# Kernel tuning notes

Hardware: AMD Instinct MI355X
Metric: run time of the kernel (lower is better)

## Reference

```python
import jax, jax.numpy as jnp
import numpy as np

B, S, D, H = 2, 2048, 2048, 16
HD = D // H
QMAX = 127.0  # 8-bit activation quant


def ste_round(x):
    # forward: round; backward: identity
    return x + jax.lax.stop_gradient(jnp.round(x) - x)


def bitlinear(x, w):
    """BitNet b1.58 linear: per-tensor ternary weights + per-token int8 activations.

    x: [..., in], w: [out, in] -> [..., out]
    """
    w_scale = jnp.maximum(jnp.mean(jnp.abs(w)), 1e-6)
    w_q = jnp.clip(ste_round(w / w_scale), -1.0, 1.0)          # ternary {-1,0,1}
    a_max = jnp.clip(jnp.max(jnp.abs(x), axis=-1, keepdims=True), 1e-8, None)
    x_q = jnp.clip(ste_round(x * (QMAX / a_max)), -QMAX, QMAX)  # int8 range
    y = jnp.einsum('bsi,oi->bso', x_q, w_q)
    return y * (w_scale * a_max / QMAX)


def setup_inputs() -> dict:
    key = jax.random.key(0)
    ks = jax.random.split(key, 5)
    std = 1.0 / np.sqrt(D)  # muP-style init from BitLinear
    return {
        'x': jax.random.normal(ks[0], (B, S, D), dtype=jnp.float32),
        'wq': jax.random.normal(ks[1], (D, D), dtype=jnp.float32) * std,
        'wk': jax.random.normal(ks[2], (D, D), dtype=jnp.float32) * std,
        'wv': jax.random.normal(ks[3], (D, D), dtype=jnp.float32) * std,
        'wo': jax.random.normal(ks[4], (D, D), dtype=jnp.float32) * std,
    }


def reference(x, wq, wk, wv, wo):
    q = bitlinear(x, wq).reshape(B, S, H, HD)
    k = bitlinear(x, wk).reshape(B, S, H, HD)
    v = bitlinear(x, wv).reshape(B, S, H, HD)
    scores = jnp.einsum('bqhd,bkhd->bhqk', q, k) / np.sqrt(HD)
    # causal mask
    causal = jnp.tril(jnp.ones((S, S), dtype=bool))
    scores = jnp.where(causal[None, None], scores, jnp.finfo(scores.dtype).min)
    attn = jax.nn.softmax(scores, axis=-1)
    ctx = jnp.einsum('bhqk,bkhd->bqhd', attn, v).reshape(B, S, D)
    return bitlinear(ctx, wo)
```

## Files before the change

kernel.cpp:

```cpp
#include <hip/hip_runtime.h>
#include <hip/hip_bf16.h>
#include <cstdint>
#include <cstddef>


#define BB 2
#define SS 2048
#define DD 2048
#define HH 16
#define HDD 128
#define MM (BB*SS)

typedef __attribute__((ext_vector_type(8))) short bf16x8;
typedef __attribute__((ext_vector_type(4))) float f32x4;
typedef __attribute__((ext_vector_type(16))) float f32x16;
typedef __attribute__((ext_vector_type(4))) int   i32x4;
typedef unsigned short u16;
typedef unsigned int   u32;
typedef unsigned char  u8;
typedef signed char    s8;

#define MFMA(a,b,c)   __builtin_amdgcn_mfma_f32_16x16x32_bf16(a,b,c,0,0,0)
#define MFMA32(a,b,c) __builtin_amdgcn_mfma_f32_32x32x16_bf16(a,b,c,0,0,0)
#define MFMAI8(a,b,c) __builtin_amdgcn_mfma_i32_16x16x64_i8(a,b,c,0,0,0)

static __device__ __forceinline__ u16 f2bf(float f) {
  u32 x = __float_as_uint(f);
  u32 r = x + 0x7fffu + ((x >> 16) & 1u);
  return (u16)(r >> 16);
}

static __device__ __forceinline__ u32 cvtpk(float a, float b) {
  u32 r;
  asm("v_cvt_pk_bf16_f32 %0, %1, %2" : "=v"(r) : "v"(a), "v"(b));
  return r;
}

static __device__ __forceinline__ void gl_lds16(const void* g, void* l) {
  __builtin_amdgcn_global_load_lds((const __attribute__((address_space(1))) void*)g,
                                   (__attribute__((address_space(3))) void*)l, 16, 0, 0);
}

__global__ __launch_bounds__(256) void k_prep(const float* __restrict__ x, s8* __restrict__ xq,
                                              float* __restrict__ amax,
                                              const float* __restrict__ w0, const float* __restrict__ w1,
                                              const float* __restrict__ w2, const float* __restrict__ w3,
                                              double* __restrict__ part) {
  __shared__ double redd[256];
  __shared__ float  redf[4];
  int t = threadIdx.x;
  if (blockIdx.x < MM) {
    int row = blockIdx.x;
    const float* p = x + (size_t)row * DD + t * 8;
    float4 v0 = *(const float4*)(p);
    float4 v1 = *(const float4*)(p + 4);
    float f[8];
    f[0] = v0.x; f[1] = v0.y; f[2] = v0.z; f[3] = v0.w;
    f[4] = v1.x; f[5] = v1.y; f[6] = v1.z; f[7] = v1.w;
    float m = 0.f;
    #pragma unroll
    for (int i = 0; i < 8; i++) m = fmaxf(m, fabsf(f[i]));
    m = fmaxf(m, __shfl_xor(m, 1));  m = fmaxf(m, __shfl_xor(m, 2));
    m = fmaxf(m, __shfl_xor(m, 4));  m = fmaxf(m, __shfl_xor(m, 8));
    m = fmaxf(m, __shfl_xor(m, 16)); m = fmaxf(m, __shfl_xor(m, 32));
    if ((t & 63) == 0) redf[t >> 6] = m;
    __syncthreads();
    m = fmaxf(fmaxf(redf[0], redf[1]), fmaxf(redf[2], redf[3]));
    m = fmaxf(m, 1e-8f);
    if (t == 0) amax[row] = m;
    float s = 127.0f / m;
    s8 o[8];
    #pragma unroll
    for (int i = 0; i < 8; i++)
      o[i] = (s8)(int)fminf(127.f, fmaxf(-127.f, rintf(f[i] * s)));
    *(uint2*)(xq + (size_t)row * DD + t * 8) = *(const uint2*)o;
  } else {
    int idx = blockIdx.x - MM;
    int m = idx >> 8, blk = idx & 255;
    const float* w = (m == 0) ? w0 : (m == 1) ? w1 : (m == 2) ? w2 : w3;
    const float* p = w + (size_t)blk * 16384;
    double s = 0.0;
    for (int i = t * 4; i < 16384; i += 1024) {
      float4 v = *(const float4*)(p + i);
      s += (double)fabsf(v.x) + (double)fabsf(v.y) + (double)fabsf(v.z) + (double)fabsf(v.w);
    }
    redd[t] = s;
    __syncthreads();
    for (int off = 128; off > 0; off >>= 1) {
      if (t < off) redd[t] += redd[t + off];
      __syncthreads();
    }
    if (t == 0) part[m * 256 + blk] = redd[0];
  }
}

__global__ void k_wscale_final(const double* __restrict__ part, float* __restrict__ scales) {
  int m = threadIdx.x;
  if (m < 4) {
    double s = 0.0;
    for (int i = 0; i < 256; i++) s += part[m * 256 + i];
    float v = (float)(s * (1.0 / 4194304.0));
    scales[m] = fmaxf(v, 1e-6f);
  }
}

__global__ void k_wquant(const float* __restrict__ w0, const float* __restrict__ w1,
                         const float* __restrict__ w2, const float* __restrict__ w3,
                         s8* __restrict__ wq, const float* __restrict__ scales) {
  int m = blockIdx.y;
  const float* w = (m == 0) ? w0 : (m == 1) ? w1 : (m == 2) ? w2 : w3;
  float ws = scales[m];
  size_t i = ((size_t)blockIdx.x * 256 + threadIdx.x) * 4;
  float4 v = *(const float4*)(w + i);
  s8 o[4];
  o[0] = (s8)(int)fminf(1.f, fmaxf(-1.f, rintf(v.x / ws)));
  o[1] = (s8)(int)fminf(1.f, fmaxf(-1.f, rintf(v.y / ws)));
  o[2] = (s8)(int)fminf(1.f, fmaxf(-1.f, rintf(v.z / ws)));
  o[3] = (s8)(int)fminf(1.f, fmaxf(-1.f, rintf(v.w / ws)));
  *(int*)(wq + (size_t)m * DD * DD + i) = *(const int*)o;
}

__global__ __launch_bounds__(256) void k_rowquant_bf(const u16* __restrict__ xin, s8* __restrict__ xq,
                                                     float* __restrict__ amax) {
  int row = blockIdx.x, t = threadIdx.x;
  const u16* p = xin + (size_t)row * DD + t * 8;
  int4 v = *(const int4*)p;
  const u16* pv = (const u16*)&v;
  float f[8];
  #pragma unroll
  for (int i = 0; i < 8; i++) f[i] = __uint_as_float((u32)pv[i] << 16);
  float m = 0.f;
  #pragma unroll
  for (int i = 0; i < 8; i++) m = fmaxf(m, fabsf(f[i]));
  m = fmaxf(m, __shfl_xor(m, 1));  m = fmaxf(m, __shfl_xor(m, 2));
  m = fmaxf(m, __shfl_xor(m, 4));  m = fmaxf(m, __shfl_xor(m, 8));
  m = fmaxf(m, __shfl_xor(m, 16)); m = fmaxf(m, __shfl_xor(m, 32));
  __shared__ float red[4];
  if ((t & 63) == 0) red[t >> 6] = m;
  __syncthreads();
  m = fmaxf(fmaxf(red[0], red[1]), fmaxf(red[2], red[3]));
  m = fmaxf(m, 1e-8f);
  if (t == 0) amax[row] = m;
  float s = 127.0f / m;
  s8 o[8];
  #pragma unroll
  for (int i = 0; i < 8; i++)
    o[i] = (s8)(int)fminf(127.f, fmaxf(-127.f, rintf(f[i] * s)));
  *(uint2*)(xq + (size_t)row * DD + t * 8) = *(const uint2*)o;
}

template<bool OB, int NBNL, int BN>
__global__ __launch_bounds__(512) void k_gemm(const s8* __restrict__ A, const s8* __restrict__ Bw,
                                              const float* __restrict__ amax,
                                              const float* __restrict__ scales, int sbase,
                                              void* __restrict__ outv) {
  constexpr int NJ = BN / 128;
  __shared__ alignas(16) u8 Asm[2][128 * 128];
  __shared__ alignas(16) u8 Bsm[2][BN * 128];
  int id = blockIdx.x;
  int xcd = id & 7, kk = id >> 3;
  int bm = kk & 31, bn = xcd * NBNL + (kk >> 5);
  int t = threadIdx.x, w = t >> 6, l = t & 63;
  int wr = w >> 2, wc = w & 3;
  int l15 = l & 15, lh = l >> 4;
  int r0 = t >> 3;
  int c0 = ((t & 7) ^ (r0 & 7)) * 16;
  const s8* Ab = A  + (size_t)(bm * 128) * DD;
  const s8* Bb = Bw + (size_t)(bn * BN) * DD;

  auto STG_A = [&](int tt) {
    u8* d_ = &Asm[tt & 1][0];
    gl_lds16(Ab + (size_t)r0 * DD + tt * 128 + c0,        d_ + t * 16);
    gl_lds16(Ab + (size_t)(r0 + 64) * DD + tt * 128 + c0, d_ + (512 + t) * 16);
  };
  auto STG_B = [&](int tt, int h_) {
    u8* d_ = &Bsm[tt & 1][(size_t)h_ * (BN / 2) * 128];
    #pragma unroll
    for (int jj = 0; jj < NJ; jj++)
      gl_lds16(Bb + (size_t)(h_ * (BN / 2) + jj * 64 + r0) * DD + tt * 128 + c0,
               d_ + (jj * 512 + t) * 16);
  };

  i32x4 acc[4][2 * NJ] = {};
  STG_A(0); STG_B(0, 0); STG_B(0, 1); STG_B(1, 0);
  if constexpr (NJ == 2) asm volatile("s_waitcnt vmcnt(2)" ::: "memory");
  else                   asm volatile("s_waitcnt vmcnt(1)" ::: "memory");
  asm volatile("s_barrier" ::: "memory");
  for (int kb = 0; kb < 16; kb++) {
    int b = kb & 1;
    const u8* Ac = &Asm[b][0];
    const u8* Bc = &Bsm[b][0];
    i32x4 af[4][2], bf[NJ][2];
    #pragma unroll
    for (int i = 0; i < 4; i++)
      #pragma unroll
      for (int ks = 0; ks < 2; ks++)
        af[i][ks] = *(const i32x4*)(Ac + (wr * 64 + i * 16 + l15) * 128 + (((ks * 4 + lh) ^ (l15 & 7)) * 16));
    #pragma unroll
    for (int j = 0; j < NJ; j++)
      #pragma unroll
      for (int ks = 0; ks < 2; ks++)
        bf[j][ks] = *(const i32x4*)(Bc + ((wc + 4 * j) * 16 + l15) * 128 + (((ks * 4 + lh) ^ (l15 & 7)) * 16));
    if (kb + 1 < 16) { STG_A(kb + 1); STG_B(kb + 1, 1); }
    asm volatile("s_barrier" ::: "memory");
    asm volatile("s_waitcnt lgkmcnt(0)" ::: "memory");
    __builtin_amdgcn_sched_barrier(0);
    __builtin_amdgcn_s_setprio(1);
    #pragma unroll
    for (int ks = 0; ks < 2; ks++)
      #pragma unroll
      for (int i = 0; i < 4; i++)
        #pragma unroll
        for (int j = 0; j < NJ; j++)
          acc[i][j] = MFMAI8(af[i][ks], bf[j][ks], acc[i][j]);
    __builtin_amdgcn_s_setprio(0);
    asm volatile("s_barrier" ::: "memory");
    i32x4 bg[NJ][2];
    #pragma unroll
    for (int j = 0; j < NJ; j++)
      #pragma unroll
      for (int ks = 0; ks < 2; ks++)
        bg[j][ks] = *(const i32x4*)(Bc + ((wc + 4 * (NJ + j)) * 16 + l15) * 128 + (((ks * 4 + lh) ^ (l15 & 7)) * 16));
    if (kb + 2 < 16) STG_B(kb + 2, 0);
    asm volatile("s_barrier" ::: "memory");
    asm volatile("s_waitcnt lgkmcnt(0)" ::: "memory");
    __builtin_amdgcn_sched_barrier(0);
    __builtin_amdgcn_s_setprio(1);
    #pragma unroll
    for (int ks = 0; ks < 2; ks++)
      #pragma unroll
      for (int i = 0; i < 4; i++)
        #pragma unroll
        for (int j = 0; j < NJ; j++)
          acc[i][NJ + j] = MFMAI8(af[i][ks], bg[j][ks], acc[i][NJ + j]);
    __builtin_amdgcn_s_setprio(0);
    if (kb < 14) {
      if constexpr (NJ == 2) asm volatile("s_waitcnt vmcnt(2)" ::: "memory");
      else                   asm volatile("s_waitcnt vmcnt(1)" ::: "memory");
      asm volatile("s_barrier" ::: "memory");
    } else if (kb == 14) {
      asm volatile("s_waitcnt vmcnt(0)" ::: "memory");
      asm volatile("s_barrier" ::: "memory");
    }
  }
  int mz = OB ? (bn >> 3) : 0;
  int lcol0 = OB ? ((bn & 7) * 256) : (bn * BN);
  float wsc = scales[sbase + mz];
  u16*   outb = (u16*)outv + (size_t)mz * MM * DD;
  float* outf = (float*)outv;
  #pragma unroll
  for (int i = 0; i < 4; i++) {
    int row0 = bm * 128 + wr * 64 + i * 16 + lh * 4;
    #pragma unroll
    for (int r = 0; r < 4; r++) {
      float sc = (wsc * amax[row0 + r]) / 127.0f;
      #pragma unroll
      for (int j = 0; j < 2 * NJ; j++) {
        int col = lcol0 + (wc + 4 * j) * 16 + l15;
        float y = (float)acc[i][j][r] * sc;
        if (OB) outb[(size_t)(row0 + r) * DD + col] = f2bf(y);
        else    outf[(size_t)(row0 + r) * DD + col] = y;
      }
    }
  }
}

__global__ __launch_bounds__(256) void k_vtrans(const u16* __restrict__ v, u16* __restrict__ vt) {
  __shared__ u16 tile[64][72];
  int sb = blockIdx.x;
  int db = blockIdx.y;
  int bh = blockIdx.z;
  int b = bh >> 4, h = bh & 15;
  int t = threadIdx.x;
  int ls = t >> 2, ld0 = (t & 3) * 16;
  const u16* src = v + (size_t)(b * SS + sb * 64 + ls) * DD + h * HDD + db * 64 + ld0;
  *(int4*)(&tile[ls][ld0])     = *(const int4*)(src);
  *(int4*)(&tile[ls][ld0 + 8]) = *(const int4*)(src + 8);
  __syncthreads();
  int d = t >> 2, s0 = (t & 3) * 16;
  u16 tmp[16];
  #pragma unroll
  for (int k = 0; k < 16; k++) tmp[k] = tile[s0 + k][d];
  u16* dst = vt + (size_t)((bh * HDD) + db * 64 + d) * SS + sb * 64 + s0;
  *(int4*)(dst)     = *(const int4*)(tmp);
  *(int4*)(dst + 8) = *(const int4*)(tmp + 8);
}

__global__ __launch_bounds__(256) void k_attn(const u16* __restrict__ Q, const u16* __restrict__ K,
                                              const u16* __restrict__ VT, u16* __restrict__ O) {
  __shared__ alignas(16) u16 Ks[2][64 * 128];
  __shared__ alignas(16) u16 Vs[2][128 * 64];
  __shared__ alignas(16) u16 Ps[4 * 32 * 64];
  int id = blockIdx.x;
  int bh = (id & 7) * 4 + ((id >> 3) & 3);
  int pr = id >> 5;
  int b = bh >> 4, h = bh & 15;
  int t = threadIdx.x, w = t >> 6, l = t & 63;
  int l31 = l & 31, hi = l >> 5;
  int l15 = l & 15, lh = l >> 4;
  size_t base = (size_t)(b * SS) * DD + h * HDD;
  const u16* vtb = VT + (size_t)bh * HDD * SS;
  u16* Ptw = Ps + w * 2048;
  const float sc2 = 0.12751944557270094f;
  int ksr[4], kso[4], vsr[4], vso[4];
  #pragma unroll
  for (int i = 0; i < 4; i++) {
    int s = i * 256 + t;
    ksr[i] = s >> 4; kso[i] = ((s & 15) ^ (ksr[i] & 15)) * 8;
    vsr[i] = s >> 3; vso[i] = ((s & 7) ^ (vsr[i] & 7)) * 8;
  }

#define ASTAGE(kb_, bf_) do {                                                           \
    _Pragma("unroll")                                                                   \
    for (int i_ = 0; i_ < 4; i_++)                                                      \
      gl_lds16(K + base + (size_t)((kb_) * 64 + ksr[i_]) * DD + kso[i_],                \
               &Ks[bf_][(i_ * 256 + t) * 8]);                                           \
    _Pragma("unroll")                                                                   \
    for (int i_ = 0; i_ < 4; i_++)                                                      \
      gl_lds16(vtb + (size_t)vsr[i_] * SS + (kb_) * 64 + vso[i_],                       \
               &Vs[bf_][(i_ * 256 + t) * 8]);                                           \
  } while (0)

  for (int half = 0; half < 2; half++) {
    int qt = half ? (15 - pr) : pr;
    int qrow = qt * 128 + w * 32 + l31;
    bf16x8 qf[8];
    #pragma unroll
    for (int kt = 0; kt < 8; kt++)
      qf[kt] = *(const bf16x8*)(Q + base + (size_t)qrow * DD + kt * 16 + hi * 8);
    f32x4 cacc[2][8] = {};
    float mrun = -INFINITY, lrun = 0.f;
    int nkb = 2 * qt + 2;
    ASTAGE(0, 0);
    asm volatile("s_waitcnt vmcnt(0)" ::: "memory");
    asm volatile("s_barrier" ::: "memory");
    for (int kb = 0; kb < nkb; kb++) {
      int cur = kb & 1;
      if (kb + 1 < nkb) ASTAGE(kb + 1, cur ^ 1);
      const u16* Kc = &Ks[cur][0];
      const u16* Vc = &Vs[cur][0];
      f32x16 c0 = {}, c1 = {};
      #pragma unroll
      for (int kt = 0; kt < 8; kt++) {
        int sl = (((kt * 2 + hi) ^ (l31 & 15)) * 8);
        bf16x8 kf0 = *(const bf16x8*)(Kc + l31 * 128 + sl);
        bf16x8 kf1 = *(const bf16x8*)(Kc + (32 + l31) * 128 + sl);
        c0 = MFMA32(kf0, qf[kt], c0);
        c1 = MFMA32(kf1, qf[kt], c1);
      }
      if (kb >= 2 * qt) {
        #pragma unroll
        for (int rg = 0; rg < 16; rg++) {
          int kv0 = kb * 64 + (rg & 3) + 8 * (rg >> 2) + 4 * hi;
          if (kv0 > qrow)      c0[rg] = -1e30f;
          if (kv0 + 32 > qrow) c1[rg] = -1e30f;
        }
      }
      float ta[16];
      #pragma unroll
      for (int rg = 0; rg < 16; rg++) ta[rg] = fmaxf(c0[rg], c1[rg]);
      #pragma unroll
      for (int off = 8; off > 0; off >>= 1)
        #pragma unroll
        for (int rg = 0; rg < 8; rg++)
          if (rg < off) ta[rg] = fmaxf(ta[rg], ta[rg + off]);
      float pmax = fmaxf(ta[0], __shfl_xor(ta[0], 32));
      if (__any(pmax - mrun > 90.50967f)) {
        float mnew = fmaxf(mrun, pmax);
        float alpha = __builtin_amdgcn_exp2f((mrun - mnew) * sc2);
        lrun *= alpha;
        #pragma unroll
        for (int m16 = 0; m16 < 2; m16++)
          #pragma unroll
          for (int r = 0; r < 4; r++) {
            float ar = __shfl(alpha, m16 * 16 + lh * 4 + r);
            #pragma unroll
            for (int n2 = 0; n2 < 8; n2++) cacc[m16][n2][r] *= ar;
          }
        mrun = mnew;
      }
      float msc2 = mrun * sc2;
      float ts[16];
      #pragma unroll
      for (int rg = 0; rg < 16; rg++) {
        float p0 = __builtin_amdgcn_exp2f(fmaf(c0[rg], sc2, -msc2)); c0[rg] = p0;
        float p1 = __builtin_amdgcn_exp2f(fmaf(c1[rg], sc2, -msc2)); c1[rg] = p1;
        ts[rg] = p0 + p1;
      }
      #pragma unroll
      for (int off = 8; off > 0; off >>= 1)
        #pragma unroll
        for (int rg = 0; rg < 8; rg++)
          if (rg < off) ts[rg] += ts[rg + off];
      lrun += ts[0] + __shfl_xor(ts[0], 32);
      #pragma unroll
      for (int q4 = 0; q4 < 4; q4++) {
        uint2 pk0, pk1;
        pk0.x = cvtpk(c0[4 * q4 + 0], c0[4 * q4 + 1]);
        pk0.y = cvtpk(c0[4 * q4 + 2], c0[4 * q4 + 3]);
        pk1.x = cvtpk(c1[4 * q4 + 0], c1[4 * q4 + 1]);
        pk1.y = cvtpk(c1[4 * q4 + 2], c1[4 * q4 + 3]);
        *(uint2*)(Ptw + l31 * 64 + ((q4 ^ (l31 & 7)) * 8 + 4 * hi))       = pk0;
        *(uint2*)(Ptw + l31 * 64 + (((4 + q4) ^ (l31 & 7)) * 8 + 4 * hi)) = pk1;
      }
      #pragma unroll
      for (int ks = 0; ks < 2; ks++) {
        int so = ((ks * 4 + lh) ^ (l15 & 7)) * 8;
        bf16x8 pf0 = *(const bf16x8*)(Ptw + (l15) * 64 + so);
        bf16x8 pf1 = *(const bf16x8*)(Ptw + (16 + l15) * 64 + so);
        #pragma unroll
        for (int n2 = 0; n2 < 8; n2++) {
          bf16x8 vf = *(const bf16x8*)(Vc + (n2 * 16 + l15) * 64 + so);
          cacc[0][n2] = MFMA(pf0, vf, cacc[0][n2]);
          cacc[1][n2] = MFMA(pf1, vf, cacc[1][n2]);
        }
      }
      asm volatile("s_waitcnt vmcnt(0)" ::: "memory");
      asm volatile("s_barrier" ::: "memory");
    }
    float inv = 1.0f / lrun;
    #pragma unroll
    for (int m16 = 0; m16 < 2; m16++)
      #pragma unroll
      for (int r = 0; r < 4; r++) {
        float ir = __shfl(inv, m16 * 16 + lh * 4 + r);
        u16* op = O + base + (size_t)(qt * 128 + w * 32 + m16 * 16 + lh * 4 + r) * DD;
        #pragma unroll
        for (int n2 = 0; n2 < 8; n2++)
          op[n2 * 16 + l15] = f2bf(cacc[m16][n2][r] * ir);
      }
  }
#undef ASTAGE
}

extern "C" void kernel_launch(void* const* d_in, const int* in_sizes, int n_in,
                              void* d_out, int out_size, void* d_ws, size_t ws_size,
                              hipStream_t stream) {
  const float* x  = (const float*)d_in[0];
  const float* wq = (const float*)d_in[1];
  const float* wk = (const float*)d_in[2];
  const float* wv = (const float*)d_in[3];
  const float* wo = (const float*)d_in[4];
  char* ws = (char*)d_ws;
  float*  scales = (float*)(ws + 0);
  double* part   = (double*)(ws + 256);
  float*  amaxx  = (float*)(ws + 16384);
  float*  amaxc  = (float*)(ws + 49152);
  s8*     wqq    = (s8*)(ws + 131072);
  s8*     xq     = (s8*)(ws + 33685504);
  u16*    vt16   = (u16*)(ws + 33685504);
  u16*    qb     = (u16*)(ws + 50462720);
  u16*    kb     = (u16*)(ws + 67239936);
  u16*    vb     = (u16*)(ws + 84017152);
  u16*    ctx    = (u16*)(ws + 100794368);
  (void)in_sizes; (void)n_in; (void)out_size; (void)ws_size;

  k_prep<<<MM + 1024, 256, 0, stream>>>(x, xq, amaxx, wq, wk, wv, wo, part);
  k_wscale_final<<<1, 64, 0, stream>>>(part, scales);
  k_wquant<<<dim3(4096, 4), 256, 0, stream>>>(wq, wk, wv, wo, wqq, scales);
  k_gemm<true, 3, 256><<<768, 512, 0, stream>>>(xq, wqq, amaxx, scales, 0, (void*)qb);
  k_vtrans<<<dim3(32, 2, 32), 256, 0, stream>>>(vb, vt16);
  k_attn<<<256, 256, 0, stream>>>(qb, kb, vt16, ctx);
  k_rowquant_bf<<<MM, 256, 0, stream>>>(ctx, xq, amaxc);
  k_gemm<false, 2, 128><<<512, 512, 0, stream>>>(xq, wqq + (size_t)3 * DD * DD, amaxc, scales, 3, d_out);
}
```

Baseline: 225.1 us.

## Split attention KV range across two blocks with flash-decoding style combine

Each attention block now processes only even or odd KV tiles, which doubles the grid from 256 to 512 blocks. Each block writes an unnormalized bf16 partial output plus its running max and sum, and a new combine kernel merges the two partials with rescaled weights into ctx. This targets underutilization, since 256 blocks cannot fill the GPU's compute units. In exchange it adds extra global traffic for the partials, a kernel launch, and a second bf16 rounding on the partial outputs.

```diff
diff --git a/kernel.cpp b/kernel.cpp
--- a/kernel.cpp
+++ b/kernel.cpp
@@ -28,6 +28,9 @@
   u32 x = __float_as_uint(f);
   u32 r = x + 0x7fffu + ((x >> 16) & 1u);
   return (u16)(r >> 16);
+}
+static __device__ __forceinline__ float bf2f(u16 v) {
+  return __uint_as_float((u32)v << 16);
 }
 
 static __device__ __forceinline__ u32 cvtpk(float a, float b) {
@@ -128,7 +131,7 @@
   const u16* pv = (const u16*)&v;
   float f[8];
   #pragma unroll
-  for (int i = 0; i < 8; i++) f[i] = __uint_as_float((u32)pv[i] << 16);
+  for (int i = 0; i < 8; i++) f[i] = bf2f(pv[i]);
   float m = 0.f;
   #pragma unroll
   for (int i = 0; i < 8; i++) m = fmaxf(m, fabsf(f[i]));
@@ -287,13 +290,17 @@
 }
 
 __global__ __launch_bounds__(256) void k_attn(const u16* __restrict__ Q, const u16* __restrict__ K,
-                                              const u16* __restrict__ VT, u16* __restrict__ O) {
+                                              const u16* __restrict__ VT,
+                                              u16* __restrict__ O0, u16* __restrict__ O1,
+                                              float2* __restrict__ ml) {
   __shared__ alignas(16) u16 Ks[2][64 * 128];
   __shared__ alignas(16) u16 Vs[2][128 * 64];
   __shared__ alignas(16) u16 Ps[4 * 32 * 64];
   int id = blockIdx.x;
   int bh = (id & 7) * 4 + ((id >> 3) & 3);
-  int pr = id >> 5;
+  int rest = id >> 5;
+  int pr = rest & 7;
+  int par = rest >> 3;
   int b = bh >> 4, h = bh & 15;
   int t = threadIdx.x, w = t >> 6, l = t & 63;
   int l31 = l & 31, hi = l >> 5;
@@ -301,6 +308,7 @@
   size_t base = (size_t)(b * SS) * DD + h * HDD;
   const u16* vtb = VT + (size_t)bh * HDD * SS;
   u16* Ptw = Ps + w * 2048;
+  u16* Opar = par ? O1 : O0;
   const float sc2 = 0.12751944557270094f;
   int ksr[4], kso[4], vsr[4], vso[4];
   #pragma unroll
@@ -331,12 +339,13 @@
     f32x4 cacc[2][8] = {};
     float mrun = -INFINITY, lrun = 0.f;
     int nkb = 2 * qt + 2;
-    ASTAGE(0, 0);
+    ASTAGE(par, 0);
     asm volatile("s_waitcnt vmcnt(0)" ::: "memory");
     asm volatile("s_barrier" ::: "memory");
-    for (int kb = 0; kb < nkb; kb++) {
-      int cur = kb & 1;
-      if (kb + 1 < nkb) ASTAGE(kb + 1, cur ^ 1);
+    int it = 0;
+    for (int kb = par; kb < nkb; kb += 2, it++) {
+      int cur = it & 1;
+      if (kb + 2 < nkb) ASTAGE(kb + 2, cur ^ 1);
       const u16* Kc = &Ks[cur][0];
       const u16* Vc = &Vs[cur][0];
       f32x16 c0 = {}, c1 = {};
@@ -418,19 +427,49 @@
       asm volatile("s_waitcnt vmcnt(0)" ::: "memory");
       asm volatile("s_barrier" ::: "memory");
     }
-    float inv = 1.0f / lrun;
+    u16* Ob = Opar + (size_t)(bh * 2048 + qt * 128) * 128;
     #pragma unroll
     for (int m16 = 0; m16 < 2; m16++)
       #pragma unroll
       for (int r = 0; r < 4; r++) {
-        float ir = __shfl(inv, m16 * 16 + lh * 4 + r);
-        u16* op = O + base + (size_t)(qt * 128 + w * 32 + m16 * 16 + lh * 4 + r) * DD;
+        u16* op = Ob + (size_t)(w * 32 + m16 * 16 + lh * 4 + r) * 128;
         #pragma unroll
         for (int n2 = 0; n2 < 8; n2++)
-          op[n2 * 16 + l15] = f2bf(cacc[m16][n2][r] * ir);
-      }
+          op[n2 * 16 + l15] = f2bf(cacc[m16][n2][r]);
+      }
+    if (l < 32) {
+      int uid = bh * 2048 + qt * 128 + w * 32 + l31;
+      ml[(size_t)par * 65536 + uid] = make_float2(mrun, lrun);
+    }
   }
 #undef ASTAGE
+}
+
+__global__ __launch_bounds__(256) void k_combine(const u16* __restrict__ O0, const u16* __restrict__ O1,
+                                                 const float2* __restrict__ ml, u16* __restrict__ ctx) {
+  const float sc2 = 0.12751944557270094f;
+  int t = threadIdx.x;
+  int unit = blockIdx.x * 16 + (t >> 4);
+  int d0 = (t & 15) * 8;
+  float2 m0 = ml[unit];
+  float2 m1 = ml[65536 + unit];
+  float m = fmaxf(m0.x, m1.x);
+  float w0 = __builtin_amdgcn_exp2f((m0.x - m) * sc2);
+  float w1 = __builtin_amdgcn_exp2f((m1.x - m) * sc2);
+  float linv = 1.0f / (w0 * m0.y + w1 * m1.y);
+  w0 *= linv; w1 *= linv;
+  int4 a = *(const int4*)(O0 + (size_t)unit * 128 + d0);
+  int4 bb = *(const int4*)(O1 + (size_t)unit * 128 + d0);
+  const u16* pa = (const u16*)&a;
+  const u16* pb = (const u16*)&bb;
+  u16 o[8];
+  #pragma unroll
+  for (int i = 0; i < 8; i++)
+    o[i] = f2bf(w0 * bf2f(pa[i]) + w1 * bf2f(pb[i]));
+  int bh = unit >> 11, qrow = unit & 2047;
+  int b = bh >> 4, h = bh & 15;
+  u16* cp = ctx + ((size_t)(b * SS + qrow)) * DD + h * HDD + d0;
+  *(int4*)cp = *(const int4*)o;
 }
 
 extern "C" void kernel_launch(void* const* d_in, const int* in_sizes, int n_in,
@@ -447,12 +486,15 @@
   float*  amaxx  = (float*)(ws + 16384);
   float*  amaxc  = (float*)(ws + 49152);
   s8*     wqq    = (s8*)(ws + 131072);
+  float2* ml     = (float2*)(ws + 16908288);
   s8*     xq     = (s8*)(ws + 33685504);
   u16*    vt16   = (u16*)(ws + 33685504);
   u16*    qb     = (u16*)(ws + 50462720);
   u16*    kb     = (u16*)(ws + 67239936);
   u16*    vb     = (u16*)(ws + 84017152);
+  u16*    O0     = (u16*)(ws + 84017152);
   u16*    ctx    = (u16*)(ws + 100794368);
+  u16*    O1     = (u16*)(ws + 117571584);
   (void)in_sizes; (void)n_in; (void)out_size; (void)ws_size;
 
   k_prep<<<MM + 1024, 256, 0, stream>>>(x, xq, amaxx, wq, wk, wv, wo, part);
@@ -460,7 +502,8 @@
   k_wquant<<<dim3(4096, 4), 256, 0, stream>>>(wq, wk, wv, wo, wqq, scales);
   k_gemm<true, 3, 256><<<768, 512, 0, stream>>>(xq, wqq, amaxx, scales, 0, (void*)qb);
   k_vtrans<<<dim3(32, 2, 32), 256, 0, stream>>>(vb, vt16);
-  k_attn<<<256, 256, 0, stream>>>(qb, kb, vt16, ctx);
+  k_attn<<<512, 256, 0, stream>>>(qb, kb, vt16, O0, O1, ml);
+  k_combine<<<4096, 256, 0, stream>>>(O0, O1, ml, ctx);
   k_rowquant_bf<<<MM, 256, 0, stream>>>(ctx, xq, amaxc);
   k_gemm<false, 2, 128><<<512, 512, 0, stream>>>(xq, wqq + (size_t)3 * DD * DD, amaxc, scales, 3, d_out);
 }
```

Result: slower. 233.2 us (+3.6%).
